# Optimization experiments

Measured on AMD Instinct MI355X. Metric: run time of the kernel, lower is better.

Reference implementation:

```python
import jax, jax.numpy as jnp
import numpy as np

N_NODES = 50000
N_GRAPHS = 512


def _glorot(key, shape):
    fan_in, fan_out = shape[0], shape[1]
    lim = float(np.sqrt(6.0 / (fan_in + fan_out)))
    return jax.random.uniform(key, shape, jnp.float32, -lim, lim)


def setup_inputs() -> dict:
    key = jax.random.key(0)
    ks = jax.random.split(key, 12)
    x = jax.random.normal(ks[0], (N_NODES, 64), jnp.float32)
    edge_index = jax.random.randint(ks[1], (2, 800000), 0, N_NODES, jnp.int64)
    batch = jnp.sort(jax.random.randint(ks[2], (N_NODES,), 0, N_GRAPHS, jnp.int64))
    # GCNConv weights stored as [in, out]; bias [out]
    W1 = _glorot(ks[3], (64, 128));  b1 = jnp.zeros((128,), jnp.float32)
    W2 = _glorot(ks[4], (128, 128)); b2 = jnp.zeros((128,), jnp.float32)
    W3 = _glorot(ks[5], (128, 64));  b3 = jnp.zeros((64,), jnp.float32)
    Wl = _glorot(ks[6], (64, 10));   bl = jnp.zeros((10,), jnp.float32)
    return {"x": x, "edge_index": edge_index, "batch": batch,
            "W1": W1, "b1": b1, "W2": W2, "b2": b2,
            "W3": W3, "b3": b3, "Wl": Wl, "bl": bl}


def _gcn_conv(h_in, W, b, row, col, dinv, n):
    # GCNConv: out = D^{-1/2} (A + I) D^{-1/2} (X W) + b, self-loops folded in
    h = h_in @ W                                   # [N, out]
    norm = (dinv[row] * dinv[col])[:, None]        # [E, 1]
    agg = jax.ops.segment_sum(h[row] * norm, col, num_segments=n)
    agg = agg + (dinv * dinv)[:, None] * h          # self-loop contribution
    return agg + b


def reference(x, edge_index, batch, W1, b1, W2, b2, W3, b3, Wl, bl):
    n = x.shape[0]
    row, col = edge_index[0], edge_index[1]
    # degree of target nodes, including self loop
    deg = jax.ops.segment_sum(jnp.ones((row.shape[0],), x.dtype), col,
                              num_segments=n) + 1.0
    dinv = deg ** -0.5

    h = jax.nn.relu(_gcn_conv(x, W1, b1, row, col, dinv, n))
    h = jax.nn.relu(_gcn_conv(h, W2, b2, row, col, dinv, n))
    h = _gcn_conv(h, W3, b3, row, col, dinv, n)

    # global mean pool over graphs
    sums = jax.ops.segment_sum(h, batch, num_segments=N_GRAPHS)
    cnts = jax.ops.segment_sum(jnp.ones((n,), h.dtype), batch,
                               num_segments=N_GRAPHS)
    pooled = sums / jnp.maximum(cnts, 1.0)[:, None]
    # dropout is identity in eval mode
    return pooled @ Wl + bl
```

## Files before the change

### kernel.cpp

```cpp
#include <hip/hip_runtime.h>
#include <hip/hip_fp16.h>

typedef _Float16 f16;
typedef f16 f16x8 __attribute__((ext_vector_type(8)));
typedef float f32x4 __attribute__((ext_vector_type(4)));


__global__ void k_zero_i32(int* __restrict__ p, int n) {
    int i = blockIdx.x * blockDim.x + threadIdx.x;
    if (i < n) p[i] = 0;
}

__global__ void k_count(const int* __restrict__ col, int E, int* __restrict__ cnt) {
    int e = blockIdx.x * blockDim.x + threadIdx.x;
    if (e < E) atomicAdd(&cnt[col[e]], 1);
}

__global__ void k_bsum(const int* __restrict__ cnt, int N, int* __restrict__ bsum) {
    __shared__ int wt[4];
    int t = threadIdx.x;
    int i0 = blockIdx.x * 1024 + t * 4;
    int s = 0;
    #pragma unroll
    for (int j = 0; j < 4; ++j) { int i = i0 + j; if (i < N) s += cnt[i]; }
    #pragma unroll
    for (int off = 32; off > 0; off >>= 1) s += __shfl_down(s, off, 64);
    if ((t & 63) == 0) wt[t >> 6] = s;
    __syncthreads();
    if (t == 0) bsum[blockIdx.x] = wt[0] + wt[1] + wt[2] + wt[3];
}

__global__ void k_bscan(int* __restrict__ bsum, int nb, int* __restrict__ starts, int N) {
    int lane = threadIdx.x;
    int carry = 0;
    for (int base = 0; base < nb; base += 64) {
        int i = base + lane;
        int v = (i < nb) ? bsum[i] : 0;
        int s = v;
        #pragma unroll
        for (int off = 1; off < 64; off <<= 1) {
            int u = __shfl_up(s, off, 64);
            if (lane >= off) s += u;
        }
        if (i < nb) bsum[i] = carry + s - v;
        carry += __shfl(s, 63, 64);
    }
    if (lane == 0) starts[N] = carry;
}

__global__ void k_scan_apply(const int* __restrict__ cnt, const int* __restrict__ bsum,
                             int* __restrict__ starts, int N) {
    __shared__ int wt[4];
    int t = threadIdx.x;
    int lane = t & 63;
    int w = t >> 6;
    int i0 = blockIdx.x * 1024 + t * 4;
    int v[4];
    int ts = 0;
    #pragma unroll
    for (int j = 0; j < 4; ++j) { int i = i0 + j; v[j] = (i < N) ? cnt[i] : 0; ts += v[j]; }
    int s = ts;
    #pragma unroll
    for (int off = 1; off < 64; off <<= 1) {
        int u = __shfl_up(s, off, 64);
        if (lane >= off) s += u;
    }
    if (lane == 63) wt[w] = s;
    __syncthreads();
    int woff = 0;
    if (w > 0) woff = wt[0];
    if (w > 1) woff += wt[1];
    if (w > 2) woff += wt[2];
    int base = bsum[blockIdx.x] + woff + (s - ts);
    int run = base;
    #pragma unroll
    for (int j = 0; j < 4; ++j) { int i = i0 + j; if (i < N) starts[i] = run; run += v[j]; }
}

__global__ void k_dinv(const int* __restrict__ starts, float* __restrict__ dinv, int N) {
    int i = blockIdx.x * blockDim.x + threadIdx.x;
    if (i < N) dinv[i] = rsqrtf((float)(starts[i + 1] - starts[i]) + 1.0f);
}

__global__ void k_fill_xcd(const int* __restrict__ row, const int* __restrict__ col, int E,
                           const int* __restrict__ starts, int* __restrict__ cnt,
                           int* __restrict__ csr, int N) {
    const int w = blockIdx.x & 7;
    const int chunk = blockIdx.x >> 3;
    const int nchunks = gridDim.x >> 3;
    const int W = (N + 7) / 8;
    const int c0 = w * W;
    const int c1 = min(N, c0 + W);
    const int stride = nchunks * blockDim.x;
    for (int e = chunk * blockDim.x + threadIdx.x; e < E; e += stride) {
        int c = col[e];
        if (c >= c0 && c < c1) {
            int pos = starts[c] + atomicSub(&cnt[c], 1) - 1;
            csr[pos] = row[e];
        }
    }
}

__global__ void k_f2h(const float* __restrict__ src, __half* __restrict__ dst, long n) {
    long i = ((long)blockIdx.x * blockDim.x + threadIdx.x) * 4;
    if (i + 3 < n) {
        float4 v = *(const float4*)&src[i];
        __half2 h0 = __floats2half2_rn(v.x, v.y);
        __half2 h1 = __floats2half2_rn(v.z, v.w);
        uint2 q; q.x = *(unsigned int*)&h0; q.y = *(unsigned int*)&h1;
        *(uint2*)&dst[i] = q;
    } else {
        for (long j = i; j < n; ++j) dst[j] = __float2half_rn(src[j]);
    }
}

__global__ void k_wprep(const float* __restrict__ W, f16* __restrict__ Wt,
                        int K, int M, int KP) {
    int idx = blockIdx.x * blockDim.x + threadIdx.x;
    if (idx >= K * M) return;
    int k = idx / M;
    int m = idx - k * M;
    Wt[(long)m * KP + k] = (f16)W[idx];
}


template<int K, int M, bool BIAS, bool RELU, typename OT>
__global__ __launch_bounds__(256) void k_gemm_mfma(const f16* __restrict__ A,
                                                   const f16* __restrict__ Wt,
                                                   const float* __restrict__ bias,
                                                   OT* __restrict__ P, int N) {
    constexpr int KP = K + 8;
    constexpr int KK = K / 32;
    __shared__ f16 Wl[M * KP];
    const int t = threadIdx.x;
    constexpr int CH = (M * KP * 2) / 16;
    {
        const uint4* src = (const uint4*)Wt;
        uint4* dst = (uint4*)Wl;
        for (int i = t; i < CH; i += 256) dst[i] = src[i];
    }
    __syncthreads();
    const int lane = t & 63;
    const int wave = t >> 6;
    const int r = lane & 15;
    const int q = lane >> 4;
    const int arow = blockIdx.x * 64 + wave * 16 + r;
    f16x8 a[KK];
    #pragma unroll
    for (int kk = 0; kk < KK; ++kk) {
        if (arow < N) a[kk] = *(const f16x8*)&A[(long)arow * K + kk * 32 + q * 8];
        else { f16x8 z = {0, 0, 0, 0, 0, 0, 0, 0}; a[kk] = z; }
    }
    const int drow0 = blockIdx.x * 64 + wave * 16 + q * 4;
    #pragma unroll
    for (int ct = 0; ct < M / 16; ++ct) {
        const int col = ct * 16 + r;
        f32x4 acc = {0.f, 0.f, 0.f, 0.f};
        #pragma unroll
        for (int kk = 0; kk < KK; ++kk) {
            f16x8 b = *(const f16x8*)&Wl[col * KP + kk * 32 + q * 8];
            acc = __builtin_amdgcn_mfma_f32_16x16x32_f16(a[kk], b, acc, 0, 0, 0);
        }
        float bb = BIAS ? bias[col] : 0.f;
        #pragma unroll
        for (int g = 0; g < 4; ++g) {
            int rr = drow0 + g;
            if (rr < N) {
                float v = acc[g] + bb;
                if (RELU) v = fmaxf(v, 0.f);
                if constexpr (__is_same(OT, f16)) P[(long)rr * M + col] = (f16)v;
                else P[(long)rr * M + col] = v;
            }
        }
    }
}


template<int M, bool BIAS, bool RELU, typename OT>
__global__ void k_agg16(const __half* __restrict__ P16, const int* __restrict__ starts,
                        const int* __restrict__ csr, const float* __restrict__ dinv,
                        const float* __restrict__ b, OT* __restrict__ H, int N) {
    constexpr int TPN = M / 8;
    constexpr int NPB = 256 / TPN;
    int local = threadIdx.x / TPN;
    int fq = threadIdx.x % TPN;
    int f0 = fq * 8;
    int c = blockIdx.x * NPB + local;
    if (c >= N) return;
    int s = starts[c], e = starts[c + 1];
    float acc[8] = {};
    int i = s;
    for (; i + 1 < e; i += 2) {
        int r0 = csr[i], r1 = csr[i + 1];
        float d0 = dinv[r0], d1 = dinv[r1];
        uint4 u0 = *(const uint4*)&P16[(long)r0 * M + f0];
        uint4 u1 = *(const uint4*)&P16[(long)r1 * M + f0];
        const __half2* h0 = (const __half2*)&u0;
        const __half2* h1 = (const __half2*)&u1;
        #pragma unroll
        for (int j = 0; j < 4; ++j) {
            float2 f0v = __half22float2(h0[j]);
            float2 f1v = __half22float2(h1[j]);
            acc[2 * j]     += f0v.x * d0 + f1v.x * d1;
            acc[2 * j + 1] += f0v.y * d0 + f1v.y * d1;
        }
    }
    if (i < e) {
        int r0 = csr[i];
        float d0 = dinv[r0];
        uint4 u0 = *(const uint4*)&P16[(long)r0 * M + f0];
        const __half2* h0 = (const __half2*)&u0;
        #pragma unroll
        for (int j = 0; j < 4; ++j) {
            float2 f0v = __half22float2(h0[j]);
            acc[2 * j]     += f0v.x * d0;
            acc[2 * j + 1] += f0v.y * d0;
        }
    }
    float dc = dinv[c];
    float dc2 = dc * dc;
    uint4 us = *(const uint4*)&P16[(long)c * M + f0];
    const __half2* hs = (const __half2*)&us;
    float v[8];
    #pragma unroll
    for (int j = 0; j < 4; ++j) {
        float2 fs = __half22float2(hs[j]);
        v[2 * j]     = dc * acc[2 * j]     + dc2 * fs.x;
        v[2 * j + 1] = dc * acc[2 * j + 1] + dc2 * fs.y;
    }
    if (BIAS) {
        float4 bb0 = *(const float4*)&b[f0];
        float4 bb1 = *(const float4*)&b[f0 + 4];
        v[0] += bb0.x; v[1] += bb0.y; v[2] += bb0.z; v[3] += bb0.w;
        v[4] += bb1.x; v[5] += bb1.y; v[6] += bb1.z; v[7] += bb1.w;
    }
    if (RELU) {
        #pragma unroll
        for (int j = 0; j < 8; ++j) v[j] = fmaxf(v[j], 0.f);
    }
    if constexpr (__is_same(OT, __half)) {
        __half2 h0 = __floats2half2_rn(v[0], v[1]);
        __half2 h1 = __floats2half2_rn(v[2], v[3]);
        __half2 h2 = __floats2half2_rn(v[4], v[5]);
        __half2 h3 = __floats2half2_rn(v[6], v[7]);
        uint4 qo;
        qo.x = *(unsigned int*)&h0; qo.y = *(unsigned int*)&h1;
        qo.z = *(unsigned int*)&h2; qo.w = *(unsigned int*)&h3;
        *(uint4*)&H[(long)c * M + f0] = qo;
    } else {
        *(float4*)&H[(long)c * M + f0]     = make_float4(v[0], v[1], v[2], v[3]);
        *(float4*)&H[(long)c * M + f0 + 4] = make_float4(v[4], v[5], v[6], v[7]);
    }
}


__global__ void k_gemm_naive(const float* __restrict__ X, const float* __restrict__ W,
                             float* __restrict__ P, int N, int K, int M) {
    long idx = (long)blockIdx.x * blockDim.x + threadIdx.x;
    long total = (long)N * M;
    if (idx >= total) return;
    int n = (int)(idx / M);
    int m = (int)(idx - (long)n * M);
    const float* xr = X + (long)n * K;
    float acc = 0.0f;
    for (int k = 0; k < K; ++k) acc += xr[k] * W[k * M + m];
    P[idx] = acc;
}

template<int M>
__global__ void k_aggregate4(const float* __restrict__ P, const int* __restrict__ starts,
                             const int* __restrict__ csr, const float* __restrict__ dinv,
                             const float* __restrict__ b, float* __restrict__ H,
                             int N, int do_relu) {
    constexpr int TPN = M / 4;
    constexpr int NPB = 256 / TPN;
    int local = threadIdx.x / TPN;
    int fq = threadIdx.x % TPN;
    int c = blockIdx.x * NPB + local;
    if (c >= N) return;
    int s = starts[c], e = starts[c + 1];
    float4 acc = make_float4(0.f, 0.f, 0.f, 0.f);
    for (int i = s; i < e; ++i) {
        int r = csr[i];
        float dr = dinv[r];
        float4 p = *(const float4*)&P[(long)r * M + fq * 4];
        acc.x += p.x * dr; acc.y += p.y * dr; acc.z += p.z * dr; acc.w += p.w * dr;
    }
    float dc = dinv[c];
    float dc2 = dc * dc;
    float4 ps = *(const float4*)&P[(long)c * M + fq * 4];
    float4 bb = *(const float4*)&b[fq * 4];
    float4 v;
    v.x = dc * acc.x + dc2 * ps.x + bb.x;
    v.y = dc * acc.y + dc2 * ps.y + bb.y;
    v.z = dc * acc.z + dc2 * ps.z + bb.z;
    v.w = dc * acc.w + dc2 * ps.w + bb.w;
    if (do_relu) {
        v.x = fmaxf(v.x, 0.f); v.y = fmaxf(v.y, 0.f);
        v.z = fmaxf(v.z, 0.f); v.w = fmaxf(v.w, 0.f);
    }
    *(float4*)&H[(long)c * M + fq * 4] = v;
}


__device__ __forceinline__ int lower_bound_i(const int* __restrict__ a, int n, int key) {
    int lo = 0, hi = n;
    while (lo < hi) { int mid = (lo + hi) >> 1; if (a[mid] < key) lo = mid + 1; else hi = mid; }
    return lo;
}

__global__ void k_pool(const float* __restrict__ H, const int* __restrict__ batch,
                       int N, int M, float* __restrict__ pooled) {
    int g = blockIdx.x;
    int f = threadIdx.x;
    int lo = lower_bound_i(batch, N, g);
    int hi = lower_bound_i(batch, N, g + 1);
    float acc = 0.0f;
    for (int n = lo; n < hi; ++n) acc += H[(long)n * M + f];
    float inv = 1.0f / fmaxf((float)(hi - lo), 1.0f);
    pooled[(long)g * M + f] = acc * inv;
}

__global__ void k_final(const float* __restrict__ pooled, const float* __restrict__ Wl,
                        const float* __restrict__ bl, float* __restrict__ out,
                        int Gn, int F, int C) {
    int idx = blockIdx.x * blockDim.x + threadIdx.x;
    if (idx >= Gn * C) return;
    int g = idx / C;
    int j = idx - g * C;
    float acc = bl[j];
    for (int f = 0; f < F; ++f) acc += pooled[g * F + f] * Wl[f * C + j];
    out[idx] = acc;
}


extern "C" void kernel_launch(void* const* d_in, const int* in_sizes, int n_in,
                              void* d_out, int out_size, void* d_ws, size_t ws_size,
                              hipStream_t stream) {
    const float* x  = (const float*)d_in[0];
    const int*   ei = (const int*)d_in[1];
    const int*   batch = (const int*)d_in[2];
    const float* W1 = (const float*)d_in[3];
    const float* b1 = (const float*)d_in[4];
    const float* W2 = (const float*)d_in[5];
    const float* b2 = (const float*)d_in[6];
    const float* W3 = (const float*)d_in[7];
    const float* b3 = (const float*)d_in[8];
    const float* Wl = (const float*)d_in[9];
    const float* bl = (const float*)d_in[10];

    const int N  = in_sizes[2];
    const int E  = in_sizes[1] / 2;
    const int C  = in_sizes[10];
    const int Gn = out_size / C;
    const int F1 = in_sizes[4];
    const int F2 = in_sizes[6];
    const int F3 = in_sizes[8];
    const int K0 = in_sizes[0] / N;

    const int* row = ei;
    const int* col = ei + E;

    char* base = (char*)d_ws;
    size_t off = 0;
    auto alloc = [&](size_t bytes) {
        off = (off + 63) & ~(size_t)63;
        void* p = base + off;
        off += bytes;
        return p;
    };
    int* cnt     = (int*)alloc((size_t)N * 4);
    int* starts  = (int*)alloc((size_t)(N + 1) * 4);
    int* bsum    = (int*)alloc(256 * 4);
    int* csr     = (int*)alloc((size_t)E * 4);
    float* dinv  = (float*)alloc((size_t)N * 4);
    __half* X16  = (__half*)alloc((size_t)N * 64 * 2);
    __half* AX16 = (__half*)alloc((size_t)N * 64 * 2);
    __half* H1   = (__half*)alloc((size_t)N * 128 * 2);
    __half* P16a = (__half*)alloc((size_t)N * 128 * 2);
    __half* B16  = (__half*)alloc((size_t)N * 128 * 2);
    __half* P16b = (__half*)alloc((size_t)N * 64 * 2);
    float* H3    = (float*)alloc((size_t)N * 64 * 4);
    f16* Wt1     = (f16*)alloc((size_t)128 * 72 * 2);
    f16* Wt2     = (f16*)alloc((size_t)128 * 136 * 2);
    f16* Wt3     = (f16*)alloc((size_t)64 * 136 * 2);
    float* pooled = (float*)alloc((size_t)Gn * 64 * 4);
    float* Afb   = (float*)alloc((size_t)N * 128 * 4);
    float* Bfb   = (float*)alloc((size_t)N * 128 * 4);

    const int BLK = 256;
    auto blocks = [](long n, int b) { return (int)((n + b - 1) / b); };
    const int nb = blocks(N, 1024);

    k_zero_i32<<<blocks(N, BLK), BLK, 0, stream>>>(cnt, N);
    k_count<<<blocks(E, BLK), BLK, 0, stream>>>(col, E, cnt);
    k_bsum<<<nb, 256, 0, stream>>>(cnt, N, bsum);
    k_bscan<<<1, 64, 0, stream>>>(bsum, nb, starts, N);
    k_scan_apply<<<nb, 256, 0, stream>>>(cnt, bsum, starts, N);
    k_dinv<<<blocks(N, BLK), BLK, 0, stream>>>(starts, dinv, N);
    k_fill_xcd<<<128 * 8, 256, 0, stream>>>(row, col, E, starts, cnt, csr, N);

    const bool fast = (K0 == 64 && F1 == 128 && F2 == 128 && F3 == 64);

    if (fast) {
        k_f2h<<<blocks(((long)N * 64 + 3) / 4, BLK), BLK, 0, stream>>>(x, X16, (long)N * 64);
        k_wprep<<<blocks(64 * 128, BLK), BLK, 0, stream>>>(W1, Wt1, 64, 128, 72);
        k_wprep<<<blocks(128 * 128, BLK), BLK, 0, stream>>>(W2, Wt2, 128, 128, 136);
        k_wprep<<<blocks(128 * 64, BLK), BLK, 0, stream>>>(W3, Wt3, 128, 64, 136);

        k_agg16<64, false, false, __half><<<blocks(N, 32), 256, 0, stream>>>(X16, starts, csr, dinv, nullptr, AX16, N);
        k_gemm_mfma<64, 128, true, true, f16><<<blocks(N, 64), 256, 0, stream>>>((const f16*)AX16, Wt1, b1, (f16*)H1, N);
        k_gemm_mfma<128, 128, false, false, f16><<<blocks(N, 64), 256, 0, stream>>>((const f16*)H1, Wt2, nullptr, (f16*)P16a, N);
        k_agg16<128, true, true, __half><<<blocks(N, 16), 256, 0, stream>>>(P16a, starts, csr, dinv, b2, B16, N);
        k_gemm_mfma<128, 64, false, false, f16><<<blocks(N, 64), 256, 0, stream>>>((const f16*)B16, Wt3, nullptr, (f16*)P16b, N);
        k_agg16<64, true, false, float><<<blocks(N, 32), 256, 0, stream>>>(P16b, starts, csr, dinv, b3, H3, N);
        k_pool<<<Gn, F3, 0, stream>>>(H3, batch, N, F3, pooled);
    } else {
        k_gemm_naive<<<blocks((long)N * F1, BLK), BLK, 0, stream>>>(x, W1, Afb, N, K0, F1);
        k_aggregate4<128><<<blocks(N, 8), 256, 0, stream>>>(Afb, starts, csr, dinv, b1, Bfb, N, 1);
        k_gemm_naive<<<blocks((long)N * F2, BLK), BLK, 0, stream>>>(Bfb, W2, Afb, N, F1, F2);
        k_aggregate4<128><<<blocks(N, 8), 256, 0, stream>>>(Afb, starts, csr, dinv, b2, Bfb, N, 1);
        k_gemm_naive<<<blocks((long)N * F3, BLK), BLK, 0, stream>>>(Bfb, W3, Afb, N, F2, F3);
        k_aggregate4<64><<<blocks(N, 16), 256, 0, stream>>>(Afb, starts, csr, dinv, b3, Bfb, N, 0);
        k_pool<<<Gn, F3, 0, stream>>>(Bfb, batch, N, F3, pooled);
    }

    k_final<<<blocks(Gn * C, BLK), BLK, 0, stream>>>(pooled, Wl, bl, (float*)d_out, Gn, F3, C);
}
```

Before: 250.1 us.

## Fuse dinv into scan, merge weight prep, unroll gather by four, fuse pool+final

Computes dinv inside the scan-apply kernel from the per-node counts, which removes a separate launch. The three weight-transpose launches become one kernel, and mean pooling is fused with the final linear layer. The aggregation gather loop is unrolled from two to four neighbors to keep more loads in flight, at the cost of more registers. Together these cut about five kernel launches and raise memory-level parallelism in the sparse gather.

```diff
diff --git a/kernel.cpp b/kernel.cpp
--- a/kernel.cpp
+++ b/kernel.cpp
@@ -49,7 +49,7 @@
 }
 
 __global__ void k_scan_apply(const int* __restrict__ cnt, const int* __restrict__ bsum,
-                             int* __restrict__ starts, int N) {
+                             int* __restrict__ starts, float* __restrict__ dinv, int N) {
     __shared__ int wt[4];
     int t = threadIdx.x;
     int lane = t & 63;
@@ -74,12 +74,14 @@
     int base = bsum[blockIdx.x] + woff + (s - ts);
     int run = base;
     #pragma unroll
-    for (int j = 0; j < 4; ++j) { int i = i0 + j; if (i < N) starts[i] = run; run += v[j]; }
-}
-
-__global__ void k_dinv(const int* __restrict__ starts, float* __restrict__ dinv, int N) {
-    int i = blockIdx.x * blockDim.x + threadIdx.x;
-    if (i < N) dinv[i] = rsqrtf((float)(starts[i + 1] - starts[i]) + 1.0f);
+    for (int j = 0; j < 4; ++j) {
+        int i = i0 + j;
+        if (i < N) {
+            starts[i] = run;
+            dinv[i] = rsqrtf((float)v[j] + 1.0f);
+        }
+        run += v[j];
+    }
 }
 
 __global__ void k_fill_xcd(const int* __restrict__ row, const int* __restrict__ col, int E,
@@ -114,13 +116,22 @@
     }
 }
 
-__global__ void k_wprep(const float* __restrict__ W, f16* __restrict__ Wt,
-                        int K, int M, int KP) {
+__global__ void k_wprep3(const float* __restrict__ W1, const float* __restrict__ W2,
+                         const float* __restrict__ W3, f16* __restrict__ Wt1,
+                         f16* __restrict__ Wt2, f16* __restrict__ Wt3) {
     int idx = blockIdx.x * blockDim.x + threadIdx.x;
-    if (idx >= K * M) return;
-    int k = idx / M;
-    int m = idx - k * M;
-    Wt[(long)m * KP + k] = (f16)W[idx];
+    if (idx < 8192) {
+        int k = idx >> 7, m = idx & 127;
+        Wt1[m * 72 + k] = (f16)W1[idx];
+    } else if (idx < 24576) {
+        int j = idx - 8192;
+        int k = j >> 7, m = j & 127;
+        Wt2[m * 136 + k] = (f16)W2[j];
+    } else if (idx < 32768) {
+        int j = idx - 24576;
+        int k = j >> 6, m = j & 63;
+        Wt3[m * 136 + k] = (f16)W3[j];
+    }
 }
 
 
@@ -190,31 +201,37 @@
     int s = starts[c], e = starts[c + 1];
     float acc[8] = {};
     int i = s;
-    for (; i + 1 < e; i += 2) {
-        int r0 = csr[i], r1 = csr[i + 1];
-        float d0 = dinv[r0], d1 = dinv[r1];
+    for (; i + 3 < e; i += 4) {
+        int r0 = csr[i], r1 = csr[i + 1], r2 = csr[i + 2], r3 = csr[i + 3];
+        float d0 = dinv[r0], d1 = dinv[r1], d2 = dinv[r2], d3 = dinv[r3];
         uint4 u0 = *(const uint4*)&P16[(long)r0 * M + f0];
         uint4 u1 = *(const uint4*)&P16[(long)r1 * M + f0];
+        uint4 u2 = *(const uint4*)&P16[(long)r2 * M + f0];
+        uint4 u3 = *(const uint4*)&P16[(long)r3 * M + f0];
         const __half2* h0 = (const __half2*)&u0;
         const __half2* h1 = (const __half2*)&u1;
+        const __half2* h2 = (const __half2*)&u2;
+        const __half2* h3 = (const __half2*)&u3;
         #pragma unroll
         for (int j = 0; j < 4; ++j) {
-            float2 f0v = __half22float2(h0[j]);
-            float2 f1v = __half22float2(h1[j]);
-            acc[2 * j]     += f0v.x * d0 + f1v.x * d1;
-            acc[2 * j + 1] += f0v.y * d0 + f1v.y * d1;
-        }
-    }
-    if (i < e) {
+            float2 v0 = __half22float2(h0[j]);
+            float2 v1 = __half22float2(h1[j]);
+            float2 v2 = __half22float2(h2[j]);
+            float2 v3 = __half22float2(h3[j]);
+            acc[2 * j]     += v0.x * d0 + v1.x * d1 + v2.x * d2 + v3.x * d3;
+            acc[2 * j + 1] += v0.y * d0 + v1.y * d1 + v2.y * d2 + v3.y * d3;
+        }
+    }
+    for (; i < e; ++i) {
         int r0 = csr[i];
         float d0 = dinv[r0];
         uint4 u0 = *(const uint4*)&P16[(long)r0 * M + f0];
         const __half2* h0 = (const __half2*)&u0;
         #pragma unroll
         for (int j = 0; j < 4; ++j) {
-            float2 f0v = __half22float2(h0[j]);
-            acc[2 * j]     += f0v.x * d0;
-            acc[2 * j + 1] += f0v.y * d0;
+            float2 v0 = __half22float2(h0[j]);
+            acc[2 * j]     += v0.x * d0;
+            acc[2 * j + 1] += v0.y * d0;
         }
     }
     float dc = dinv[c];
@@ -307,6 +324,26 @@
     int lo = 0, hi = n;
     while (lo < hi) { int mid = (lo + hi) >> 1; if (a[mid] < key) lo = mid + 1; else hi = mid; }
     return lo;
+}
+
+__global__ void k_poolfinal(const float* __restrict__ H, const int* __restrict__ batch,
+                            int N, const float* __restrict__ Wl,
+                            const float* __restrict__ bl, float* __restrict__ out, int C) {
+    __shared__ float pl[64];
+    int g = blockIdx.x;
+    int f = threadIdx.x;
+    int lo = lower_bound_i(batch, N, g);
+    int hi = lower_bound_i(batch, N, g + 1);
+    float acc = 0.0f;
+    for (int n = lo; n < hi; ++n) acc += H[(long)n * 64 + f];
+    pl[f] = acc / fmaxf((float)(hi - lo), 1.0f);
+    __syncthreads();
+    if (f < C) {
+        float o = bl[f];
+        #pragma unroll 8
+        for (int k = 0; k < 64; ++k) o += pl[k] * Wl[k * C + f];
+        out[g * C + f] = o;
+    }
 }
 
 __global__ void k_pool(const float* __restrict__ H, const int* __restrict__ batch,
@@ -396,17 +433,14 @@
     k_count<<<blocks(E, BLK), BLK, 0, stream>>>(col, E, cnt);
     k_bsum<<<nb, 256, 0, stream>>>(cnt, N, bsum);
     k_bscan<<<1, 64, 0, stream>>>(bsum, nb, starts, N);
-    k_scan_apply<<<nb, 256, 0, stream>>>(cnt, bsum, starts, N);
-    k_dinv<<<blocks(N, BLK), BLK, 0, stream>>>(starts, dinv, N);
+    k_scan_apply<<<nb, 256, 0, stream>>>(cnt, bsum, starts, dinv, N);
     k_fill_xcd<<<128 * 8, 256, 0, stream>>>(row, col, E, starts, cnt, csr, N);
 
     const bool fast = (K0 == 64 && F1 == 128 && F2 == 128 && F3 == 64);
 
     if (fast) {
         k_f2h<<<blocks(((long)N * 64 + 3) / 4, BLK), BLK, 0, stream>>>(x, X16, (long)N * 64);
-        k_wprep<<<blocks(64 * 128, BLK), BLK, 0, stream>>>(W1, Wt1, 64, 128, 72);
-        k_wprep<<<blocks(128 * 128, BLK), BLK, 0, stream>>>(W2, Wt2, 128, 128, 136);
-        k_wprep<<<blocks(128 * 64, BLK), BLK, 0, stream>>>(W3, Wt3, 128, 64, 136);
+        k_wprep3<<<128, 256, 0, stream>>>(W1, W2, W3, Wt1, Wt2, Wt3);
 
         k_agg16<64, false, false, __half><<<blocks(N, 32), 256, 0, stream>>>(X16, starts, csr, dinv, nullptr, AX16, N);
         k_gemm_mfma<64, 128, true, true, f16><<<blocks(N, 64), 256, 0, stream>>>((const f16*)AX16, Wt1, b1, (f16*)H1, N);
@@ -414,7 +448,7 @@
         k_agg16<128, true, true, __half><<<blocks(N, 16), 256, 0, stream>>>(P16a, starts, csr, dinv, b2, B16, N);
         k_gemm_mfma<128, 64, false, false, f16><<<blocks(N, 64), 256, 0, stream>>>((const f16*)B16, Wt3, nullptr, (f16*)P16b, N);
         k_agg16<64, true, false, float><<<blocks(N, 32), 256, 0, stream>>>(P16b, starts, csr, dinv, b3, H3, N);
-        k_pool<<<Gn, F3, 0, stream>>>(H3, batch, N, F3, pooled);
+        k_poolfinal<<<Gn, 64, 0, stream>>>(H3, batch, N, Wl, bl, (float*)d_out, C);
     } else {
         k_gemm_naive<<<blocks((long)N * F1, BLK), BLK, 0, stream>>>(x, W1, Afb, N, K0, F1);
         k_aggregate4<128><<<blocks(N, 8), 256, 0, stream>>>(Afb, starts, csr, dinv, b1, Bfb, N, 1);
@@ -423,7 +457,6 @@
         k_gemm_naive<<<blocks((long)N * F3, BLK), BLK, 0, stream>>>(Bfb, W3, Afb, N, F2, F3);
         k_aggregate4<64><<<blocks(N, 16), 256, 0, stream>>>(Afb, starts, csr, dinv, b3, Bfb, N, 0);
         k_pool<<<Gn, F3, 0, stream>>>(Bfb, batch, N, F3, pooled);
-    }
-
-    k_final<<<blocks(Gn * C, BLK), BLK, 0, stream>>>(pooled, Wl, bl, (float*)d_out, Gn, F3, C);
-}
+        k_final<<<blocks(Gn * C, BLK), BLK, 0, stream>>>(pooled, Wl, bl, (float*)d_out, Gn, F3, C);
+    }
+}
```

After: 231.4 us. -7.4%, faster.
